# Kernel tuning notes

Measured on AMD Instinct MI355X. Metric: run time of the kernel, lower is better.

## Reference

```python
import jax, jax.numpy as jnp
import numpy as np

N = 100000
E = 640000
H = 128
C = 16


def setup_inputs() -> dict:
    key = jax.random.key(0)
    ks = jax.random.split(key, 8)
    s = 1.0 / np.sqrt(H)
    return {
        "x": jax.random.normal(ks[0], (N, H), dtype=jnp.float32),
        "edge_index": jax.random.randint(ks[1], (2, E), 0, N, dtype=jnp.int64),
        "W1l": jax.random.uniform(ks[2], (H, H), jnp.float32, -s, s),
        "W1r": jax.random.uniform(ks[3], (H, H), jnp.float32, -s, s),
        "b1": jnp.zeros((H,), jnp.float32),
        "W2l": jax.random.uniform(ks[4], (H, C), jnp.float32, -s, s),
        "W2r": jax.random.uniform(ks[5], (H, C), jnp.float32, -s, s),
        "b2": jnp.zeros((C,), jnp.float32),
    }


def sage_conv(x, src, dst, Wl, Wr, b):
    # mean aggregation of source-node features onto destination nodes
    msg_sum = jax.ops.segment_sum(x[src], dst, num_segments=N)      # [N, d]
    deg = jax.ops.segment_sum(jnp.ones((src.shape[0],), x.dtype), dst, num_segments=N)
    agg = msg_sum / jnp.maximum(deg, 1.0)[:, None]
    # lin_l(agg) + lin_r(x); bias lives in lin_l (PyG SAGEConv default)
    return agg @ Wl + x @ Wr + b


def reference(x, edge_index, W1l, W1r, b1, W2l, W2r, b2):
    src, dst = edge_index[0], edge_index[1]
    h = sage_conv(x, src, dst, W1l, W1r, b1)
    h = jax.nn.relu(h)
    # F.dropout in eval mode == identity (reference run in eval)
    out = sage_conv(h, src, dst, W2l, W2r, b2)
    return out
```

## Files before the change

kernel.cpp:

```cpp
#include <hip/hip_runtime.h>

#define NNODES 100000
#define NEDGES 640000
#define HDIM 128
#define CDIM 16
#define NP 100352
#define SLOTS 32

typedef __attribute__((ext_vector_type(8))) short bf16x8;
typedef __attribute__((ext_vector_type(4))) float f32x4;

union U16x8 { uint4 u; bf16x8 v; };

__device__ __forceinline__ unsigned short f2bf(float f) {
    unsigned int u = __float_as_uint(f);
    unsigned int r = (u + 0x7fffu + ((u >> 16) & 1u)) >> 16;
    return (unsigned short)r;
}
__device__ __forceinline__ float bf2f(unsigned short s) {
    return __uint_as_float(((unsigned int)s) << 16);
}

__device__ __forceinline__ void acc8(float (&a)[8], uint4 u) {
    a[0] += bf2f(u.x & 0xffff); a[1] += bf2f(u.x >> 16);
    a[2] += bf2f(u.y & 0xffff); a[3] += bf2f(u.y >> 16);
    a[4] += bf2f(u.z & 0xffff); a[5] += bf2f(u.z >> 16);
    a[6] += bf2f(u.w & 0xffff); a[7] += bf2f(u.w >> 16);
}

__global__ __launch_bounds__(256) void binfuse_kernel(
    const int* __restrict__ src, const int* __restrict__ dst,
    int* __restrict__ cnt, int* __restrict__ ebuf,
    const float* __restrict__ x, unsigned short* __restrict__ xb,
    const float* __restrict__ W1l, const float* __restrict__ W1r,
    const float* __restrict__ W2l, const float* __restrict__ W2r,
    unsigned short* __restrict__ w1img, unsigned short* __restrict__ w2img)
{
    const int b = blockIdx.x;
    const int tid = threadIdx.x;
    const int m5 = b % 5;

    int d = 0, s = 0, p = SLOTS;
    if (m5 == 0) {
        int e = (b / 5) * 256 + tid;
        d = dst[e];
        s = src[e];
        p = atomicAdd(&cnt[d], 1);
    }

    {
        int i = b * 256 + tid;
        float4 v = reinterpret_cast<const float4*>(x)[i];
        ushort4 r;
        r.x = f2bf(v.x); r.y = f2bf(v.y); r.z = f2bf(v.z); r.w = f2bf(v.w);
        reinterpret_cast<ushort4*>(xb)[i] = r;
    }

    if (m5 == 0) {
        if (p < SLOTS) ebuf[d * SLOTS + p] = s;
    } else if (m5 == 1 && b < 5 * 144) {
        int idx = (b / 5) * 256 + tid;
        if (idx < 32768) {
            int n = idx >> 8;
            int k = idx & 255;
            int half = k >> 7;
            int kk = k & 127;
            float v = half ? W1r[kk * HDIM + n] : W1l[kk * HDIM + n];
            int ck = kk >> 3;
            w1img[half * 16384 + n * 128 + ((ck ^ (n & 7)) << 3) + (kk & 7)] = f2bf(v);
        } else {
            int rem = idx - 32768;
            int n = rem >> 7;
            int k = rem & 127;
            float v = (n < 16) ? W2l[k * CDIM + n] : W2r[k * CDIM + (n - 16)];
            int ck = k >> 3;
            w2img[n * 128 + ((ck ^ (n & 7)) << 3) + (k & 7)] = f2bf(v);
        }
    }
}

__global__ __launch_bounds__(512, 6) void gemm_fused_kernel(
    const unsigned short* __restrict__ xb, const int* __restrict__ cnt,
    const int* __restrict__ ebuf,
    const unsigned short* __restrict__ w1img, const unsigned short* __restrict__ w2img,
    const float* __restrict__ b1, const float* __restrict__ b2,
    float* __restrict__ pq)
{
    __shared__ alignas(16) unsigned short LW[128 * 128];
    __shared__ alignas(16) unsigned short W2s[32 * 128];

    const int tid = threadIdx.x;
    const int wave = tid >> 6;
    const int lane = tid & 63;
    const int lm = lane & 15;
    const int lq = lane >> 4;
    const int row0 = blockIdx.x * 128;
    const int row = row0 + wave * 16 + lm;
    const bool valid = row < NNODES;

    {
        const uint4* wsrc = reinterpret_cast<const uint4*>(w1img);
        uint4* wdst = reinterpret_cast<uint4*>(LW);
        #pragma unroll
        for (int j = 0; j < 4; ++j) wdst[tid + j * 512] = wsrc[tid + j * 512];
    }

    const uint4* xbv = reinterpret_cast<const uint4*>(xb);

    float ag[4][8];
    #pragma unroll
    for (int kt = 0; kt < 4; ++kt) {
        #pragma unroll
        for (int i = 0; i < 8; ++i) ag[kt][i] = 0.0f;
    }
    int deg = 0;
    if (valid) {
        deg = cnt[row];
        int n = min(deg, SLOTS);
        const int* eb = ebuf + row * SLOTS;
        int j = 0;
        for (; j + 1 < n; j += 2) {
            int2 ss = *reinterpret_cast<const int2*>(eb + j);
            size_t b0 = (size_t)ss.x * 16 + lq;
            size_t b1v = (size_t)ss.y * 16 + lq;
            #pragma unroll
            for (int kt = 0; kt < 4; ++kt) {
                uint4 u = xbv[b0 + kt * 4];
                uint4 v = xbv[b1v + kt * 4];
                acc8(ag[kt], u);
                acc8(ag[kt], v);
            }
        }
        if (j < n) {
            int s0 = eb[j];
            size_t b0 = (size_t)s0 * 16 + lq;
            #pragma unroll
            for (int kt = 0; kt < 4; ++kt) acc8(ag[kt], xbv[b0 + kt * 4]);
        }
    }
    const float sc = 1.0f / fmaxf((float)deg, 1.0f);

    U16x8 af[8];
    #pragma unroll
    for (int kt = 0; kt < 4; ++kt) {
        uint4 r;
        r.x = (unsigned)f2bf(ag[kt][0] * sc) | ((unsigned)f2bf(ag[kt][1] * sc) << 16);
        r.y = (unsigned)f2bf(ag[kt][2] * sc) | ((unsigned)f2bf(ag[kt][3] * sc) << 16);
        r.z = (unsigned)f2bf(ag[kt][4] * sc) | ((unsigned)f2bf(ag[kt][5] * sc) << 16);
        r.w = (unsigned)f2bf(ag[kt][6] * sc) | ((unsigned)f2bf(ag[kt][7] * sc) << 16);
        af[kt].u = r;
    }
    {
        uint4 z = make_uint4(0u, 0u, 0u, 0u);
        size_t abase = (size_t)row * 16 + lq;
        #pragma unroll
        for (int kt = 0; kt < 4; ++kt) af[4 + kt].u = valid ? xbv[abase + kt * 4] : z;
    }

    float bv[8];
    #pragma unroll
    for (int ct = 0; ct < 8; ++ct) bv[ct] = b1[ct * 16 + lm];
    const float bq = b2[lm];

    f32x4 acc[8];
    #pragma unroll
    for (int c = 0; c < 8; ++c) acc[c] = (f32x4)(0.0f);

    __syncthreads();

    #pragma unroll
    for (int kt = 0; kt < 4; ++kt) {
        int c = kt * 4 + lq;
        #pragma unroll
        for (int ct = 0; ct < 8; ++ct) {
            int n = ct * 16 + lm;
            bf16x8 bfrag = *reinterpret_cast<const bf16x8*>(&LW[n * 128 + ((c ^ (n & 7)) << 3)]);
            acc[ct] = __builtin_amdgcn_mfma_f32_16x16x32_bf16(af[kt].v, bfrag, acc[ct], 0, 0, 0);
        }
    }
    __syncthreads();

    {
        const uint4* wsrc = reinterpret_cast<const uint4*>(w1img + 16384);
        uint4* wdst = reinterpret_cast<uint4*>(LW);
        #pragma unroll
        for (int j = 0; j < 4; ++j) wdst[tid + j * 512] = wsrc[tid + j * 512];
        uint4 w = reinterpret_cast<const uint4*>(w2img)[tid];
        reinterpret_cast<uint4*>(W2s)[tid] = w;
    }
    __syncthreads();

    #pragma unroll
    for (int kt = 0; kt < 4; ++kt) {
        int c = kt * 4 + lq;
        #pragma unroll
        for (int ct = 0; ct < 8; ++ct) {
            int n = ct * 16 + lm;
            bf16x8 bfrag = *reinterpret_cast<const bf16x8*>(&LW[n * 128 + ((c ^ (n & 7)) << 3)]);
            acc[ct] = __builtin_amdgcn_mfma_f32_16x16x32_bf16(af[4 + kt].v, bfrag, acc[ct], 0, 0, 0);
        }
    }
    __syncthreads();

    #pragma unroll
    for (int i = 0; i < 4; ++i) {
        int r = wave * 16 + lq * 4 + i;
        #pragma unroll
        for (int ct = 0; ct < 8; ++ct) {
            int c = ct * 16 + lm;
            float v = fmaxf(acc[ct][i] + bv[ct], 0.0f);
            LW[r * 128 + (((c >> 3) ^ (r & 7)) << 3) + (c & 7)] = f2bf(v);
        }
    }
    __syncthreads();

    {
        const int arow = wave * 16 + lm;

        U16x8 a2[4];
        #pragma unroll
        for (int kt = 0; kt < 4; ++kt) {
            int ck = kt * 4 + lq;
            a2[kt].v = *reinterpret_cast<const bf16x8*>(&LW[arow * 128 + ((ck ^ (arow & 7)) << 3)]);
        }

        f32x4 acc2[2];
        acc2[0] = (f32x4)(0.0f);
        acc2[1] = (f32x4)(0.0f);

        #pragma unroll
        for (int kt = 0; kt < 4; ++kt) {
            int c = kt * 4 + lq;
            #pragma unroll
            for (int ct = 0; ct < 2; ++ct) {
                int n = ct * 16 + lm;
                bf16x8 bfrag = *reinterpret_cast<const bf16x8*>(&W2s[n * 128 + ((c ^ (n & 7)) << 3)]);
                acc2[ct] = __builtin_amdgcn_mfma_f32_16x16x32_bf16(a2[kt].v, bfrag, acc2[ct], 0, 0, 0);
            }
        }

        #pragma unroll
        for (int ct = 0; ct < 2; ++ct) {
            int col = ct * 16 + lm;
            float bvv = (ct == 1) ? bq : 0.0f;
            #pragma unroll
            for (int i = 0; i < 4; ++i) {
                int r = row0 + wave * 16 + lq * 4 + i;
                if (r < NNODES)
                    pq[(size_t)r * 32 + col] = acc2[ct][i] + bvv;
            }
        }
    }
}

__global__ __launch_bounds__(256) void gather2_kernel(
    const float* __restrict__ pq, const int* __restrict__ cnt,
    const int* __restrict__ ebuf, float* __restrict__ out)
{
    int t = blockIdx.x * blockDim.x + threadIdx.x;
    int node = t >> 2;
    int c = t & 3;
    if (node >= NNODES) return;
    int deg = cnt[node];
    int n = min(deg, SLOTS);
    const int* eb = ebuf + node * SLOTS;
    float ax = 0.f, ay = 0.f, az = 0.f, aw = 0.f;
    int j = 0;
    for (; j + 1 < n; j += 2) {
        int2 ss = *reinterpret_cast<const int2*>(eb + j);
        float4 v0 = reinterpret_cast<const float4*>(pq)[ss.x * 8 + c];
        float4 v1 = reinterpret_cast<const float4*>(pq)[ss.y * 8 + c];
        ax += v0.x + v1.x; ay += v0.y + v1.y; az += v0.z + v1.z; aw += v0.w + v1.w;
    }
    if (j < n) {
        int s0 = eb[j];
        float4 v0 = reinterpret_cast<const float4*>(pq)[s0 * 8 + c];
        ax += v0.x; ay += v0.y; az += v0.z; aw += v0.w;
    }
    float sc = 1.0f / fmaxf((float)deg, 1.0f);
    float4 q = reinterpret_cast<const float4*>(pq)[node * 8 + 4 + c];
    float4 r;
    r.x = ax * sc + q.x; r.y = ay * sc + q.y; r.z = az * sc + q.z; r.w = aw * sc + q.w;
    reinterpret_cast<float4*>(out)[node * 4 + c] = r;
}

extern "C" void kernel_launch(void* const* d_in, const int* in_sizes, int n_in,
                              void* d_out, int out_size, void* d_ws, size_t ws_size,
                              hipStream_t stream) {
    const float* x   = (const float*)d_in[0];
    const int*   ei  = (const int*)d_in[1];
    const float* W1l = (const float*)d_in[2];
    const float* W1r = (const float*)d_in[3];
    const float* b1  = (const float*)d_in[4];
    const float* W2l = (const float*)d_in[5];
    const float* W2r = (const float*)d_in[6];
    const float* b2  = (const float*)d_in[7];
    float* out = (float*)d_out;

    const int* src = ei;
    const int* dst = ei + NEDGES;

    int* cnt  = (int*)d_ws;
    int* ebuf = cnt + NP;
    unsigned short* xb  = (unsigned short*)(ebuf + (size_t)NNODES * SLOTS);
    float* pq = (float*)(xb + (size_t)NNODES * HDIM);
    unsigned short* w1img = (unsigned short*)(pq + (size_t)NNODES * 32);
    unsigned short* w2img = w1img + 32768;

    hipMemsetAsync(cnt, 0, NP * sizeof(int), stream);

    binfuse_kernel<<<12500, 256, 0, stream>>>(src, dst, cnt, ebuf, x, xb,
                                              W1l, W1r, W2l, W2r, w1img, w2img);

    int ntiles1 = (NNODES + 127) / 128;
    gemm_fused_kernel<<<ntiles1, 512, 0, stream>>>(xb, cnt, ebuf, w1img, w2img, b1, b2, pq);

    gather2_kernel<<<(NNODES * 4 + 255) / 256, 256, 0, stream>>>(pq, cnt, ebuf, out);
}
```

Baseline: 212.8 us.

## Halve GEMM tile to 64 rows and stream W1 through LDS in quarters

The fused aggregation+GEMM kernel now uses 256-thread blocks covering 64 rows instead of 512-thread blocks covering 128 rows. The LDS weight buffer is halved, and W1 is staged in four 64-column chunks with extra barriers between them. Loading of the self-feature A fragments is deferred until after the aggregated half is consumed, which cuts live registers. The aim is higher occupancy and better latency hiding for the irregular neighbor gather. The cost is that each row pays twice the weight traffic from L2 and there are more synchronizations.

```diff
diff --git a/kernel.cpp b/kernel.cpp
--- a/kernel.cpp
+++ b/kernel.cpp
@@ -79,14 +79,14 @@
     }
 }
 
-__global__ __launch_bounds__(512, 6) void gemm_fused_kernel(
+__global__ __launch_bounds__(256, 4) void gemm_fused_kernel(
     const unsigned short* __restrict__ xb, const int* __restrict__ cnt,
     const int* __restrict__ ebuf,
     const unsigned short* __restrict__ w1img, const unsigned short* __restrict__ w2img,
     const float* __restrict__ b1, const float* __restrict__ b2,
     float* __restrict__ pq)
 {
-    __shared__ alignas(16) unsigned short LW[128 * 128];
+    __shared__ alignas(16) unsigned short LW[64 * 128];
     __shared__ alignas(16) unsigned short W2s[32 * 128];
 
     const int tid = threadIdx.x;
@@ -94,16 +94,15 @@
     const int lane = tid & 63;
     const int lm = lane & 15;
     const int lq = lane >> 4;
-    const int row0 = blockIdx.x * 128;
+    const int row0 = blockIdx.x * 64;
     const int row = row0 + wave * 16 + lm;
     const bool valid = row < NNODES;
 
-    {
-        const uint4* wsrc = reinterpret_cast<const uint4*>(w1img);
-        uint4* wdst = reinterpret_cast<uint4*>(LW);
-        #pragma unroll
-        for (int j = 0; j < 4; ++j) wdst[tid + j * 512] = wsrc[tid + j * 512];
-    }
+    const uint4* w1v = reinterpret_cast<const uint4*>(w1img);
+    uint4* lwv = reinterpret_cast<uint4*>(LW);
+
+    #pragma unroll
+    for (int j = 0; j < 4; ++j) lwv[tid + j * 256] = w1v[tid + j * 256];
 
     const uint4* xbv = reinterpret_cast<const uint4*>(xb);
 
@@ -140,7 +139,7 @@
     }
     const float sc = 1.0f / fmaxf((float)deg, 1.0f);
 
-    U16x8 af[8];
+    U16x8 af[4];
     #pragma unroll
     for (int kt = 0; kt < 4; ++kt) {
         uint4 r;
@@ -150,54 +149,81 @@
         r.w = (unsigned)f2bf(ag[kt][6] * sc) | ((unsigned)f2bf(ag[kt][7] * sc) << 16);
         af[kt].u = r;
     }
+
+    float bv[8];
+    #pragma unroll
+    for (int ct = 0; ct < 8; ++ct) bv[ct] = b1[ct * 16 + lm];
+    const float bq = b2[lm];
+
+    f32x4 acc[8];
+    #pragma unroll
+    for (int c = 0; c < 8; ++c) acc[c] = (f32x4)(0.0f);
+
+    __syncthreads();
+
+    #pragma unroll
+    for (int kt = 0; kt < 4; ++kt) {
+        int c = kt * 4 + lq;
+        #pragma unroll
+        for (int ct = 0; ct < 4; ++ct) {
+            int nl = ct * 16 + lm;
+            bf16x8 bfrag = *reinterpret_cast<const bf16x8*>(&LW[nl * 128 + ((c ^ (lm & 7)) << 3)]);
+            acc[ct] = __builtin_amdgcn_mfma_f32_16x16x32_bf16(af[kt].v, bfrag, acc[ct], 0, 0, 0);
+        }
+    }
+    __syncthreads();
+    #pragma unroll
+    for (int j = 0; j < 4; ++j) lwv[tid + j * 256] = w1v[1024 + tid + j * 256];
+    __syncthreads();
+
+    #pragma unroll
+    for (int kt = 0; kt < 4; ++kt) {
+        int c = kt * 4 + lq;
+        #pragma unroll
+        for (int ct = 4; ct < 8; ++ct) {
+            int nl = (ct - 4) * 16 + lm;
+            bf16x8 bfrag = *reinterpret_cast<const bf16x8*>(&LW[nl * 128 + ((c ^ (lm & 7)) << 3)]);
+            acc[ct] = __builtin_amdgcn_mfma_f32_16x16x32_bf16(af[kt].v, bfrag, acc[ct], 0, 0, 0);
+        }
+    }
+    __syncthreads();
+    {
+        #pragma unroll
+        for (int j = 0; j < 4; ++j) lwv[tid + j * 256] = w1v[2048 + tid + j * 256];
+        reinterpret_cast<uint4*>(W2s)[tid]       = reinterpret_cast<const uint4*>(w2img)[tid];
+        reinterpret_cast<uint4*>(W2s)[tid + 256] = reinterpret_cast<const uint4*>(w2img)[tid + 256];
+    }
     {
         uint4 z = make_uint4(0u, 0u, 0u, 0u);
         size_t abase = (size_t)row * 16 + lq;
         #pragma unroll
-        for (int kt = 0; kt < 4; ++kt) af[4 + kt].u = valid ? xbv[abase + kt * 4] : z;
-    }
-
-    float bv[8];
-    #pragma unroll
-    for (int ct = 0; ct < 8; ++ct) bv[ct] = b1[ct * 16 + lm];
-    const float bq = b2[lm];
-
-    f32x4 acc[8];
-    #pragma unroll
-    for (int c = 0; c < 8; ++c) acc[c] = (f32x4)(0.0f);
-
+        for (int kt = 0; kt < 4; ++kt) af[kt].u = valid ? xbv[abase + kt * 4] : z;
+    }
     __syncthreads();
 
     #pragma unroll
     for (int kt = 0; kt < 4; ++kt) {
         int c = kt * 4 + lq;
         #pragma unroll
-        for (int ct = 0; ct < 8; ++ct) {
-            int n = ct * 16 + lm;
-            bf16x8 bfrag = *reinterpret_cast<const bf16x8*>(&LW[n * 128 + ((c ^ (n & 7)) << 3)]);
+        for (int ct = 0; ct < 4; ++ct) {
+            int nl = ct * 16 + lm;
+            bf16x8 bfrag = *reinterpret_cast<const bf16x8*>(&LW[nl * 128 + ((c ^ (lm & 7)) << 3)]);
             acc[ct] = __builtin_amdgcn_mfma_f32_16x16x32_bf16(af[kt].v, bfrag, acc[ct], 0, 0, 0);
         }
     }
     __syncthreads();
-
-    {
-        const uint4* wsrc = reinterpret_cast<const uint4*>(w1img + 16384);
-        uint4* wdst = reinterpret_cast<uint4*>(LW);
-        #pragma unroll
-        for (int j = 0; j < 4; ++j) wdst[tid + j * 512] = wsrc[tid + j * 512];
-        uint4 w = reinterpret_cast<const uint4*>(w2img)[tid];
-        reinterpret_cast<uint4*>(W2s)[tid] = w;
-    }
+    #pragma unroll
+    for (int j = 0; j < 4; ++j) lwv[tid + j * 256] = w1v[3072 + tid + j * 256];
     __syncthreads();
 
     #pragma unroll
     for (int kt = 0; kt < 4; ++kt) {
         int c = kt * 4 + lq;
         #pragma unroll
-        for (int ct = 0; ct < 8; ++ct) {
-            int n = ct * 16 + lm;
-            bf16x8 bfrag = *reinterpret_cast<const bf16x8*>(&LW[n * 128 + ((c ^ (n & 7)) << 3)]);
-            acc[ct] = __builtin_amdgcn_mfma_f32_16x16x32_bf16(af[4 + kt].v, bfrag, acc[ct], 0, 0, 0);
+        for (int ct = 4; ct < 8; ++ct) {
+            int nl = (ct - 4) * 16 + lm;
+            bf16x8 bfrag = *reinterpret_cast<const bf16x8*>(&LW[nl * 128 + ((c ^ (lm & 7)) << 3)]);
+            acc[ct] = __builtin_amdgcn_mfma_f32_16x16x32_bf16(af[kt].v, bfrag, acc[ct], 0, 0, 0);
         }
     }
     __syncthreads();
@@ -312,8 +338,8 @@
     binfuse_kernel<<<12500, 256, 0, stream>>>(src, dst, cnt, ebuf, x, xb,
                                               W1l, W1r, W2l, W2r, w1img, w2img);
 
-    int ntiles1 = (NNODES + 127) / 128;
-    gemm_fused_kernel<<<ntiles1, 512, 0, stream>>>(xb, cnt, ebuf, w1img, w2img, b1, b2, pq);
+    int ntiles1 = (NNODES + 63) / 64;
+    gemm_fused_kernel<<<ntiles1, 256, 0, stream>>>(xb, cnt, ebuf, w1img, w2img, b1, b2, pq);
 
     gather2_kernel<<<(NNODES * 4 + 255) / 256, 256, 0, stream>>>(pq, cnt, ebuf, out);
 }
```

Result: faster. 186.9 us (-12.1%).

## Split layer-1 GEMM phases to cut register use and unroll layer-2 gather

Applied to the files above, without the earlier changes.

Changes the fused GEMM kernel so the self-feature (x) fragments are loaded only after the aggregated-feature MFMA pass, reusing one 4-entry fragment array instead of eight. W2 is now staged to LDS at kernel start, and the launch-bounds occupancy hint drops from 6 to 4. This lowers register pressure but fewer waves are requested. The second gather kernel also gets a 4-wide unrolled neighbor loop with int4 index loads, putting more loads in flight per thread.

```diff
diff --git a/kernel.cpp b/kernel.cpp
--- a/kernel.cpp
+++ b/kernel.cpp
@@ -79,7 +79,7 @@
     }
 }
 
-__global__ __launch_bounds__(512, 6) void gemm_fused_kernel(
+__global__ __launch_bounds__(512, 4) void gemm_fused_kernel(
     const unsigned short* __restrict__ xb, const int* __restrict__ cnt,
     const int* __restrict__ ebuf,
     const unsigned short* __restrict__ w1img, const unsigned short* __restrict__ w2img,
@@ -98,12 +98,12 @@
     const int row = row0 + wave * 16 + lm;
     const bool valid = row < NNODES;
 
-    {
-        const uint4* wsrc = reinterpret_cast<const uint4*>(w1img);
-        uint4* wdst = reinterpret_cast<uint4*>(LW);
-        #pragma unroll
-        for (int j = 0; j < 4; ++j) wdst[tid + j * 512] = wsrc[tid + j * 512];
-    }
+    const uint4* w1v = reinterpret_cast<const uint4*>(w1img);
+    uint4* lwv = reinterpret_cast<uint4*>(LW);
+
+    #pragma unroll
+    for (int j = 0; j < 4; ++j) lwv[tid + j * 512] = w1v[tid + j * 512];
+    reinterpret_cast<uint4*>(W2s)[tid] = reinterpret_cast<const uint4*>(w2img)[tid];
 
     const uint4* xbv = reinterpret_cast<const uint4*>(xb);
 
@@ -140,7 +140,7 @@
     }
     const float sc = 1.0f / fmaxf((float)deg, 1.0f);
 
-    U16x8 af[8];
+    U16x8 af[4];
     #pragma unroll
     for (int kt = 0; kt < 4; ++kt) {
         uint4 r;
@@ -150,22 +150,38 @@
         r.w = (unsigned)f2bf(ag[kt][6] * sc) | ((unsigned)f2bf(ag[kt][7] * sc) << 16);
         af[kt].u = r;
     }
+
+    float bv[8];
+    #pragma unroll
+    for (int ct = 0; ct < 8; ++ct) bv[ct] = b1[ct * 16 + lm];
+    const float bq = b2[lm];
+
+    f32x4 acc[8];
+    #pragma unroll
+    for (int c = 0; c < 8; ++c) acc[c] = (f32x4)(0.0f);
+
+    __syncthreads();
+
+    #pragma unroll
+    for (int kt = 0; kt < 4; ++kt) {
+        int c = kt * 4 + lq;
+        #pragma unroll
+        for (int ct = 0; ct < 8; ++ct) {
+            int nl = ct * 16 + lm;
+            bf16x8 bfrag = *reinterpret_cast<const bf16x8*>(&LW[nl * 128 + ((c ^ (lm & 7)) << 3)]);
+            acc[ct] = __builtin_amdgcn_mfma_f32_16x16x32_bf16(af[kt].v, bfrag, acc[ct], 0, 0, 0);
+        }
+    }
+    __syncthreads();
+
+    #pragma unroll
+    for (int j = 0; j < 4; ++j) lwv[tid + j * 512] = w1v[2048 + tid + j * 512];
     {
         uint4 z = make_uint4(0u, 0u, 0u, 0u);
         size_t abase = (size_t)row * 16 + lq;
         #pragma unroll
-        for (int kt = 0; kt < 4; ++kt) af[4 + kt].u = valid ? xbv[abase + kt * 4] : z;
-    }
-
-    float bv[8];
-    #pragma unroll
-    for (int ct = 0; ct < 8; ++ct) bv[ct] = b1[ct * 16 + lm];
-    const float bq = b2[lm];
-
-    f32x4 acc[8];
-    #pragma unroll
-    for (int c = 0; c < 8; ++c) acc[c] = (f32x4)(0.0f);
-
+        for (int kt = 0; kt < 4; ++kt) af[kt].u = valid ? xbv[abase + kt * 4] : z;
+    }
     __syncthreads();
 
     #pragma unroll
@@ -173,31 +189,9 @@
         int c = kt * 4 + lq;
         #pragma unroll
         for (int ct = 0; ct < 8; ++ct) {
-            int n = ct * 16 + lm;
-            bf16x8 bfrag = *reinterpret_cast<const bf16x8*>(&LW[n * 128 + ((c ^ (n & 7)) << 3)]);
+            int nl = ct * 16 + lm;
+            bf16x8 bfrag = *reinterpret_cast<const bf16x8*>(&LW[nl * 128 + ((c ^ (lm & 7)) << 3)]);
             acc[ct] = __builtin_amdgcn_mfma_f32_16x16x32_bf16(af[kt].v, bfrag, acc[ct], 0, 0, 0);
-        }
-    }
-    __syncthreads();
-
-    {
-        const uint4* wsrc = reinterpret_cast<const uint4*>(w1img + 16384);
-        uint4* wdst = reinterpret_cast<uint4*>(LW);
-        #pragma unroll
-        for (int j = 0; j < 4; ++j) wdst[tid + j * 512] = wsrc[tid + j * 512];
-        uint4 w = reinterpret_cast<const uint4*>(w2img)[tid];
-        reinterpret_cast<uint4*>(W2s)[tid] = w;
-    }
-    __syncthreads();
-
-    #pragma unroll
-    for (int kt = 0; kt < 4; ++kt) {
-        int c = kt * 4 + lq;
-        #pragma unroll
-        for (int ct = 0; ct < 8; ++ct) {
-            int n = ct * 16 + lm;
-            bf16x8 bfrag = *reinterpret_cast<const bf16x8*>(&LW[n * 128 + ((c ^ (n & 7)) << 3)]);
-            acc[ct] = __builtin_amdgcn_mfma_f32_16x16x32_bf16(af[4 + kt].v, bfrag, acc[ct], 0, 0, 0);
         }
     }
     __syncthreads();
@@ -264,21 +258,33 @@
     int deg = cnt[node];
     int n = min(deg, SLOTS);
     const int* eb = ebuf + node * SLOTS;
+    const float4* pqv = reinterpret_cast<const float4*>(pq);
     float ax = 0.f, ay = 0.f, az = 0.f, aw = 0.f;
     int j = 0;
+    for (; j + 3 < n; j += 4) {
+        int4 ss = *reinterpret_cast<const int4*>(eb + j);
+        float4 v0 = pqv[ss.x * 8 + c];
+        float4 v1 = pqv[ss.y * 8 + c];
+        float4 v2 = pqv[ss.z * 8 + c];
+        float4 v3 = pqv[ss.w * 8 + c];
+        ax += (v0.x + v1.x) + (v2.x + v3.x);
+        ay += (v0.y + v1.y) + (v2.y + v3.y);
+        az += (v0.z + v1.z) + (v2.z + v3.z);
+        aw += (v0.w + v1.w) + (v2.w + v3.w);
+    }
     for (; j + 1 < n; j += 2) {
         int2 ss = *reinterpret_cast<const int2*>(eb + j);
-        float4 v0 = reinterpret_cast<const float4*>(pq)[ss.x * 8 + c];
-        float4 v1 = reinterpret_cast<const float4*>(pq)[ss.y * 8 + c];
+        float4 v0 = pqv[ss.x * 8 + c];
+        float4 v1 = pqv[ss.y * 8 + c];
         ax += v0.x + v1.x; ay += v0.y + v1.y; az += v0.z + v1.z; aw += v0.w + v1.w;
     }
     if (j < n) {
         int s0 = eb[j];
-        float4 v0 = reinterpret_cast<const float4*>(pq)[s0 * 8 + c];
+        float4 v0 = pqv[s0 * 8 + c];
         ax += v0.x; ay += v0.y; az += v0.z; aw += v0.w;
     }
     float sc = 1.0f / fmaxf((float)deg, 1.0f);
-    float4 q = reinterpret_cast<const float4*>(pq)[node * 8 + 4 + c];
+    float4 q = pqv[node * 8 + 4 + c];
     float4 r;
     r.x = ax * sc + q.x; r.y = ay * sc + q.y; r.z = az * sc + q.z; r.w = aw * sc + q.w;
     reinterpret_cast<float4*>(out)[node * 4 + c] = r;
```

Result: faster. 193.3 us (-9.1%).
